# Kernel tuning notes

Hardware: AMD Instinct MI355X
Metric: run time of the kernel (lower is better)

The kernel has to match this reference:

```python
import jax, jax.numpy as jnp
import numpy as np

N_LAYERS = 2
N_ENT = 50000


def setup_inputs() -> dict:
    key = jax.random.key(0)
    k1, k2, k3, k4, k5 = jax.random.split(key, 5)
    R, N, D, E = 16, N_ENT, 128, 50000
    return {
        "ent_emb": jax.random.normal(k1, (N, D), dtype=jnp.float32),
        "rel_trans": jax.random.normal(k2, (R, D, D), dtype=jnp.float32) * (1.0 / np.sqrt(D)),
        "edge_val": jax.random.uniform(k3, (R, E), dtype=jnp.float32),
        "edge_row": jax.random.randint(k4, (R, E), 0, N, dtype=jnp.int32),
        "edge_col": jax.random.randint(k5, (R, E), 0, N, dtype=jnp.int32),
    }


def _spmm(row, col, val, emb):
    # out[i] = sum_{edges e with row[e]==i} val[e] * emb[col[e]]  (A @ emb)
    msgs = emb[col] * val[:, None]            # [E, d]
    return jax.ops.segment_sum(msgs, row, num_segments=N_ENT)  # [N, d]


def reference(ent_emb, rel_trans, edge_val, edge_row, edge_col):
    emb = ent_emb
    for _ in range(N_LAYERS):
        # per-relation sparse A_r @ emb -> [R, N, d]
        emb_acc = jax.vmap(_spmm, in_axes=(0, 0, 0, None))(edge_row, edge_col, edge_val, emb)
        # batched relation transform: rel_trans[r] @ emb_acc[r].T, transposed back
        tmp = jnp.einsum("rij,rnj->rni", rel_trans, emb_acc)  # [R, N, d]
        emb = jax.nn.relu(jnp.sum(tmp, axis=0))               # [N, d]
    # F.normalize: L2 along dim=1 with eps=1e-12
    norm = jnp.linalg.norm(emb, axis=1, keepdims=True)
    emb = emb / jnp.maximum(norm, 1e-12)
    return emb
```

## Files before the change

### kernel.cpp

```cpp
#include <hip/hip_runtime.h>
#include <stdint.h>

#define NE 50000
#define DD 128
#define RR 16
#define EE 50000
#define NT 64
#define NTOT (RR * NE)
#define SCAN_BLK 4096
#define NSCAN ((NTOT + SCAN_BLK - 1) / SCAN_BLK)

typedef short  shortx8 __attribute__((ext_vector_type(8)));
typedef short  shortx4 __attribute__((ext_vector_type(4)));
typedef float  floatx4 __attribute__((ext_vector_type(4)));

__device__ __forceinline__ unsigned short f2bf(float f) {
    unsigned u = __float_as_uint(f);
    u += 0x7fffu + ((u >> 16) & 1u);
    return (unsigned short)(u >> 16);
}
__device__ __forceinline__ float bf2f(unsigned short h) {
    return __uint_as_float(((unsigned)h) << 16);
}

#define ZB 782
#define TB 128
#define EB 6250
__global__ void prep_k(const float* __restrict__ rt, unsigned short* __restrict__ Tf,
                       const float4* __restrict__ emb, shortx4* __restrict__ embA,
                       int* __restrict__ counts) {
    int b = blockIdx.x, t = threadIdx.x;
    if (b < ZB) {
        int i4 = b * 256 + t;
        if (i4 < NTOT / 4) *(int4*)(counts + i4 * 4) = make_int4(0, 0, 0, 0);
    } else if (b < ZB + TB) {
        int c = (b - ZB) * 256 + t;
        int r = c >> 11, row = (c >> 4) & 127, cb = c & 15;
        int kt = cb >> 2, qq = cb & 3, rg = row >> 4, m = row & 15;
        const float4* src = (const float4*)(rt + (size_t)c * 8);
        float4 v0 = src[0], v1 = src[1];
        shortx8 w;
        w[0] = (short)f2bf(v0.x); w[1] = (short)f2bf(v0.y);
        w[2] = (short)f2bf(v0.z); w[3] = (short)f2bf(v0.w);
        w[4] = (short)f2bf(v1.x); w[5] = (short)f2bf(v1.y);
        w[6] = (short)f2bf(v1.z); w[7] = (short)f2bf(v1.w);
        size_t idx = ((((size_t)r * 8 + rg) * 4 + kt) * 64 + qq * 16 + m) * 8;
        *(shortx8*)(Tf + idx) = w;
    } else {
        int i = (b - ZB - TB) * 256 + t;
        if (i < NE * DD / 4) {
            float4 v = emb[i];
            shortx4 w;
            w[0] = (short)f2bf(v.x); w[1] = (short)f2bf(v.y);
            w[2] = (short)f2bf(v.z); w[3] = (short)f2bf(v.w);
            embA[i] = w;
        }
    }
}

__global__ void hist_k(const int* __restrict__ erow, int* __restrict__ counts,
                       uchar4* __restrict__ rank) {
    int r  = blockIdx.y;
    int i4 = blockIdx.x * 256 + threadIdx.x;
    if (i4 < EE / 4) {
        int4 rw = *(const int4*)(erow + (size_t)r * EE + i4 * 4);
        uchar4 rk;
        rk.x = (unsigned char)atomicAdd(&counts[rw.x * RR + r], 1);
        rk.y = (unsigned char)atomicAdd(&counts[rw.y * RR + r], 1);
        rk.z = (unsigned char)atomicAdd(&counts[rw.z * RR + r], 1);
        rk.w = (unsigned char)atomicAdd(&counts[rw.w * RR + r], 1);
        rank[(size_t)r * (EE / 4) + i4] = rk;
    }
}

__global__ void scanA(const int* __restrict__ c, int* __restrict__ bsum) {
    int b = blockIdx.x, t = threadIdx.x;
    int base = b * SCAN_BLK + t * 16;
    int s = 0;
    #pragma unroll
    for (int i = 0; i < 16; i++) {
        int idx = base + i;
        if (idx < NTOT) s += c[idx];
    }
    __shared__ int sh[256];
    sh[t] = s;
    __syncthreads();
    for (int off = 128; off > 0; off >>= 1) {
        if (t < off) sh[t] += sh[t + off];
        __syncthreads();
    }
    if (t == 0) bsum[b] = sh[0];
}

__global__ void scanC(const int* __restrict__ counts, int* __restrict__ rp,
                      const int* __restrict__ bsum) {
    int b = blockIdx.x, t = threadIdx.x;
    __shared__ int shb[256];
    shb[t] = (t < NSCAN) ? bsum[t] : 0;
    __syncthreads();
    for (int off = 1; off < 256; off <<= 1) {
        int add = (t >= off) ? shb[t - off] : 0;
        __syncthreads();
        shb[t] += add;
        __syncthreads();
    }
    int blockPrefix = (b > 0) ? shb[b - 1] : 0;
    int base = b * SCAN_BLK + t * 16;
    int vals[16];
    int s = 0;
    #pragma unroll
    for (int i = 0; i < 16; i++) {
        int idx = base + i;
        vals[i] = (idx < NTOT) ? counts[idx] : 0;
        s += vals[i];
    }
    __shared__ int sh[256];
    sh[t] = s;
    __syncthreads();
    for (int off = 1; off < 256; off <<= 1) {
        int add = (t >= off) ? sh[t - off] : 0;
        __syncthreads();
        sh[t] += add;
        __syncthreads();
    }
    int run = blockPrefix + sh[t] - s;
    #pragma unroll
    for (int i = 0; i < 16; i++) {
        int idx = base + i;
        if (idx < NTOT) {
            rp[idx] = run;
            run += vals[i];
            if (idx == NTOT - 1) rp[NTOT] = run;
        }
    }
}

__global__ void fill_k(const int* __restrict__ erow, const int* __restrict__ ecol,
                       const float* __restrict__ eval, const int* __restrict__ rp,
                       const uchar4* __restrict__ rank, int2* __restrict__ edges) {
    int r  = blockIdx.y;
    int i4 = blockIdx.x * 256 + threadIdx.x;
    if (i4 < EE / 4) {
        int4   rw = *(const int4*)(erow + (size_t)r * EE + i4 * 4);
        int4   cl = *(const int4*)(ecol + (size_t)r * EE + i4 * 4);
        float4 vl = *(const float4*)(eval + (size_t)r * EE + i4 * 4);
        uchar4 rk = rank[(size_t)r * (EE / 4) + i4];
        edges[rp[rw.x * RR + r] + rk.x] = make_int2(cl.x, __float_as_int(vl.x));
        edges[rp[rw.y * RR + r] + rk.y] = make_int2(cl.y, __float_as_int(vl.y));
        edges[rp[rw.z * RR + r] + rk.z] = make_int2(cl.z, __float_as_int(vl.z));
        edges[rp[rw.w * RR + r] + rk.w] = make_int2(cl.w, __float_as_int(vl.w));
    }
}

__device__ __forceinline__ void accum_chunks(float a0[8], float a1[8], float v,
                                             shortx8 c0, shortx8 c1) {
    #pragma unroll
    for (int j = 0; j < 8; j++) {
        a0[j] = fmaf(v, bf2f((unsigned short)c0[j]), a0[j]);
        a1[j] = fmaf(v, bf2f((unsigned short)c1[j]), a1[j]);
    }
}

template<bool FINAL>
__global__ __launch_bounds__(256, 4)
void layer_k(const unsigned short* __restrict__ embIn,
             const unsigned short* __restrict__ Tf,
             const int* __restrict__ rp,
             const int2* __restrict__ eg,
             unsigned short* __restrict__ embOut,
             float* __restrict__ outF)
{
    __shared__ __align__(16) unsigned short Bt[64 * 128];
    __shared__ float ssred[4][64];

    const int t    = threadIdx.x;
    const int lane = t & 63;
    const int w    = t >> 6;
    const int colq = lane & 15;
    const int q    = lane >> 4;
    const int n0   = blockIdx.x * NT;
    const int nsub = t >> 3;
    const int dgrp = t & 7;

    floatx4 acc[2][4];
    #pragma unroll
    for (int a = 0; a < 2; a++)
        #pragma unroll
        for (int c = 0; c < 4; c++)
            acc[a][c] = (floatx4){0.f, 0.f, 0.f, 0.f};

    #pragma unroll 1
    for (int r = 0; r < RR; r++) {
        int s_[2], c_[2];
        #pragma unroll
        for (int p = 0; p < 2; p++) {
            int n = n0 + p * 32 + nsub;
            bool ok = n < NE;
            int key = (ok ? n : 0) * RR + r;
            int a = rp[key], b2 = rp[key + 1];
            s_[p] = a; c_[p] = ok ? (b2 - a) : 0;
        }
        int   col0[2], col1[2];
        float v0_[2], v1_[2];
        #pragma unroll
        for (int p = 0; p < 2; p++) {
            int2 E0 = eg[s_[p]];
            int2 E1 = eg[s_[p] + 1];
            col0[p] = c_[p] > 0 ? E0.x : 0;
            col1[p] = c_[p] > 1 ? E1.x : 0;
            v0_[p]  = c_[p] > 0 ? __int_as_float(E0.y) : 0.f;
            v1_[p]  = c_[p] > 1 ? __int_as_float(E1.y) : 0.f;
        }
        shortx8 m[2][2][2];
        #pragma unroll
        for (int p = 0; p < 2; p++) {
            const unsigned short* r0 = embIn + (size_t)col0[p] * DD + dgrp * 8;
            const unsigned short* r1 = embIn + (size_t)col1[p] * DD + dgrp * 8;
            m[p][0][0] = *(const shortx8*)r0;
            m[p][0][1] = *(const shortx8*)(r0 + 64);
            m[p][1][0] = *(const shortx8*)r1;
            m[p][1][1] = *(const shortx8*)(r1 + 64);
        }
        #pragma unroll
        for (int p = 0; p < 2; p++) {
            float a0[8], a1[8];
            #pragma unroll
            for (int j = 0; j < 8; j++) { a0[j] = 0.f; a1[j] = 0.f; }
            accum_chunks(a0, a1, v0_[p], m[p][0][0], m[p][0][1]);
            accum_chunks(a0, a1, v1_[p], m[p][1][0], m[p][1][1]);
            if (c_[p] > 2) {
                #pragma unroll 1
                for (int k = s_[p] + 2; k < s_[p] + c_[p]; k++) {
                    int2 E = eg[k];
                    float v = __int_as_float(E.y);
                    const unsigned short* rw_ = embIn + (size_t)E.x * DD + dgrp * 8;
                    accum_chunks(a0, a1, v, *(const shortx8*)rw_, *(const shortx8*)(rw_ + 64));
                }
            }
            int nl = p * 32 + nsub;
            shortx8 w0, w1;
            #pragma unroll
            for (int j = 0; j < 8; j++) { w0[j] = (short)f2bf(a0[j]); w1[j] = (short)f2bf(a1[j]); }
            int pc = (dgrp ^ nl) & 7;
            *(shortx8*)&Bt[nl * 128 + pc * 8] = w0;
            *(shortx8*)&Bt[nl * 128 + (8 | pc) * 8] = w1;
        }
        __syncthreads();

        shortx8 afN[2];
        #pragma unroll
        for (int it2 = 0; it2 < 2; it2++)
            afN[it2] = *(const shortx8*)(Tf + ((((size_t)r * 8 + (w * 2 + it2)) * 4 + 0) * 64 + lane) * 8);
        #pragma unroll 1
        for (int kt = 0; kt < 4; kt++) {
            shortx8 afC[2];
            afC[0] = afN[0]; afC[1] = afN[1];
            if (kt < 3) {
                #pragma unroll
                for (int it2 = 0; it2 < 2; it2++)
                    afN[it2] = *(const shortx8*)(Tf + ((((size_t)r * 8 + (w * 2 + it2)) * 4 + (kt + 1)) * 64 + lane) * 8);
            }
            int lc = kt * 4 + q;
            shortx8 bfr[4];
            #pragma unroll
            for (int c = 0; c < 4; c++) {
                int nl = c * 16 + colq;
                int pc = (lc & 8) | ((lc ^ nl) & 7);
                bfr[c] = *(const shortx8*)&Bt[nl * 128 + pc * 8];
            }
            #pragma unroll
            for (int it2 = 0; it2 < 2; it2++)
                #pragma unroll
                for (int c = 0; c < 4; c++)
                    acc[it2][c] = __builtin_amdgcn_mfma_f32_16x16x32_bf16(afC[it2], bfr[c], acc[it2][c], 0, 0, 0);
        }
        __syncthreads();
    }

    if (!FINAL) {
        #pragma unroll
        for (int c = 0; c < 4; c++) {
            int n = n0 + c * 16 + colq;
            if (n < NE) {
                #pragma unroll
                for (int it2 = 0; it2 < 2; it2++) {
                    shortx4 wv;
                    #pragma unroll
                    for (int g = 0; g < 4; g++) {
                        float v = acc[it2][c][g];
                        v = v > 0.f ? v : 0.f;
                        wv[g] = (short)f2bf(v);
                    }
                    *(shortx4*)(embOut + ((size_t)n * DD + w * 32 + it2 * 16 + q * 4)) = wv;
                }
            }
        }
    } else {
        #pragma unroll
        for (int c = 0; c < 4; c++) {
            float ss = 0.f;
            #pragma unroll
            for (int it2 = 0; it2 < 2; it2++)
                #pragma unroll
                for (int g = 0; g < 4; g++) {
                    float v = acc[it2][c][g];
                    v = v > 0.f ? v : 0.f;
                    acc[it2][c][g] = v;
                    ss += v * v;
                }
            ss += __shfl_xor(ss, 16, 64);
            ss += __shfl_xor(ss, 32, 64);
            if (q == 0) ssred[w][c * 16 + colq] = ss;
        }
        __syncthreads();
        #pragma unroll
        for (int c = 0; c < 4; c++) {
            int nl = c * 16 + colq;
            float tot = ssred[0][nl] + ssred[1][nl] + ssred[2][nl] + ssred[3][nl];
            float scale = 1.f / fmaxf(sqrtf(tot), 1e-12f);
            int n = n0 + nl;
            if (n < NE) {
                #pragma unroll
                for (int it2 = 0; it2 < 2; it2++) {
                    floatx4 v4;
                    #pragma unroll
                    for (int g = 0; g < 4; g++) v4[g] = acc[it2][c][g] * scale;
                    *(floatx4*)(outF + ((size_t)n * DD + w * 32 + it2 * 16 + q * 4)) = v4;
                }
            }
        }
    }
}

static inline size_t align256(size_t x) { return (x + 255) & ~(size_t)255; }

extern "C" void kernel_launch(void* const* d_in, const int* in_sizes, int n_in,
                              void* d_out, int out_size, void* d_ws, size_t ws_size,
                              hipStream_t stream)
{
    const float* ent_emb   = (const float*)d_in[0];
    const float* rel_trans = (const float*)d_in[1];
    const float* edge_val  = (const float*)d_in[2];
    const int*   edge_row  = (const int*)d_in[3];
    const int*   edge_col  = (const int*)d_in[4];
    float* out = (float*)d_out;

    char* ws = (char*)d_ws;
    size_t off = 0;
    int* counts = (int*)(ws + off);  off = align256(off + (size_t)NTOT * 4);
    int* rpf    = (int*)(ws + off);  off = align256(off + ((size_t)NTOT + 1) * 4);
    int* bsum   = (int*)(ws + off);  off = align256(off + 256 * 4);
    uchar4* rank = (uchar4*)(ws + off); off = align256(off + (size_t)NTOT);
    int2* edges = (int2*)(ws + off); off = align256(off + ((size_t)NTOT + 4) * 8);
    unsigned short* Tf   = (unsigned short*)(ws + off); off = align256(off + (size_t)RR * DD * DD * 2);
    unsigned short* embA = (unsigned short*)(ws + off); off = align256(off + (size_t)NE * DD * 2);
    unsigned short* embB = (unsigned short*)(ws + off); off = align256(off + (size_t)NE * DD * 2);

    prep_k<<<ZB + TB + EB, 256, 0, stream>>>(rel_trans, Tf, (const float4*)ent_emb,
                                             (shortx4*)embA, counts);
    dim3 eg_grid((EE / 4 + 255) / 256, RR);
    hist_k<<<eg_grid, 256, 0, stream>>>(edge_row, counts, rank);
    scanA<<<NSCAN, 256, 0, stream>>>(counts, bsum);
    scanC<<<NSCAN, 256, 0, stream>>>(counts, rpf, bsum);
    fill_k<<<eg_grid, 256, 0, stream>>>(edge_row, edge_col, edge_val, rpf, rank, edges);

    int nb = (NE + NT - 1) / NT;
    layer_k<false><<<nb, 256, 0, stream>>>(embA, Tf, rpf, edges, embB, nullptr);
    layer_k<true ><<<nb, 256, 0, stream>>>(embB, Tf, rpf, edges, nullptr, out);
}
```

Measured before the change: 330.9 us.

## Double-buffer LDS tile and overlap next relation's gather with MFMA phase

Double-buffers the shared Bt tile so the sparse gather/accumulate for relation r+1 runs while the MFMA transform for relation r executes. Edge metadata is prefetched two relations ahead, and the first four edges per row are loaded up front instead of two. One barrier per iteration replaces two. Doubling LDS and lowering launch bounds to 3 blocks per SM reduces occupancy and raises register pressure in exchange for latency hiding.

```diff
diff --git a/kernel.cpp b/kernel.cpp
--- a/kernel.cpp
+++ b/kernel.cpp
@@ -162,7 +162,7 @@
 }
 
 template<bool FINAL>
-__global__ __launch_bounds__(256, 4)
+__global__ __launch_bounds__(256, 3)
 void layer_k(const unsigned short* __restrict__ embIn,
              const unsigned short* __restrict__ Tf,
              const int* __restrict__ rp,
@@ -170,7 +170,7 @@
              unsigned short* __restrict__ embOut,
              float* __restrict__ outF)
 {
-    __shared__ __align__(16) unsigned short Bt[64 * 128];
+    __shared__ __align__(16) unsigned short Bt[2][64 * 128];
     __shared__ float ssred[4][64];
 
     const int t    = threadIdx.x;
@@ -189,64 +189,39 @@
         for (int c = 0; c < 4; c++)
             acc[a][c] = (floatx4){0.f, 0.f, 0.f, 0.f};
 
-    #pragma unroll 1
-    for (int r = 0; r < RR; r++) {
-        int s_[2], c_[2];
+    struct EdgeMeta { int s[2], c[2]; int2 e0[2], e1[2]; };
+
+    auto metaEg = [&](int rr, EdgeMeta& st) {
         #pragma unroll
         for (int p = 0; p < 2; p++) {
             int n = n0 + p * 32 + nsub;
             bool ok = n < NE;
-            int key = (ok ? n : 0) * RR + r;
+            int key = (ok ? n : 0) * RR + rr;
             int a = rp[key], b2 = rp[key + 1];
-            s_[p] = a; c_[p] = ok ? (b2 - a) : 0;
-        }
-        int   col0[2], col1[2];
-        float v0_[2], v1_[2];
+            st.s[p] = a; st.c[p] = ok ? (b2 - a) : 0;
+            st.e0[p] = eg[a];
+            st.e1[p] = eg[a + 1];
+        }
+    };
+
+    auto embIssue = [&](const EdgeMeta& st, shortx8 (&mm)[2][2][2], float (&vv)[2][2]) {
         #pragma unroll
         for (int p = 0; p < 2; p++) {
-            int2 E0 = eg[s_[p]];
-            int2 E1 = eg[s_[p] + 1];
-            col0[p] = c_[p] > 0 ? E0.x : 0;
-            col1[p] = c_[p] > 1 ? E1.x : 0;
-            v0_[p]  = c_[p] > 0 ? __int_as_float(E0.y) : 0.f;
-            v1_[p]  = c_[p] > 1 ? __int_as_float(E1.y) : 0.f;
-        }
-        shortx8 m[2][2][2];
-        #pragma unroll
-        for (int p = 0; p < 2; p++) {
-            const unsigned short* r0 = embIn + (size_t)col0[p] * DD + dgrp * 8;
-            const unsigned short* r1 = embIn + (size_t)col1[p] * DD + dgrp * 8;
-            m[p][0][0] = *(const shortx8*)r0;
-            m[p][0][1] = *(const shortx8*)(r0 + 64);
-            m[p][1][0] = *(const shortx8*)r1;
-            m[p][1][1] = *(const shortx8*)(r1 + 64);
-        }
-        #pragma unroll
-        for (int p = 0; p < 2; p++) {
-            float a0[8], a1[8];
-            #pragma unroll
-            for (int j = 0; j < 8; j++) { a0[j] = 0.f; a1[j] = 0.f; }
-            accum_chunks(a0, a1, v0_[p], m[p][0][0], m[p][0][1]);
-            accum_chunks(a0, a1, v1_[p], m[p][1][0], m[p][1][1]);
-            if (c_[p] > 2) {
-                #pragma unroll 1
-                for (int k = s_[p] + 2; k < s_[p] + c_[p]; k++) {
-                    int2 E = eg[k];
-                    float v = __int_as_float(E.y);
-                    const unsigned short* rw_ = embIn + (size_t)E.x * DD + dgrp * 8;
-                    accum_chunks(a0, a1, v, *(const shortx8*)rw_, *(const shortx8*)(rw_ + 64));
-                }
-            }
-            int nl = p * 32 + nsub;
-            shortx8 w0, w1;
-            #pragma unroll
-            for (int j = 0; j < 8; j++) { w0[j] = (short)f2bf(a0[j]); w1[j] = (short)f2bf(a1[j]); }
-            int pc = (dgrp ^ nl) & 7;
-            *(shortx8*)&Bt[nl * 128 + pc * 8] = w0;
-            *(shortx8*)&Bt[nl * 128 + (8 | pc) * 8] = w1;
-        }
-        __syncthreads();
-
+            int col0 = st.c[p] > 0 ? st.e0[p].x : 0;
+            int col1 = st.c[p] > 1 ? st.e1[p].x : 0;
+            vv[p][0] = st.c[p] > 0 ? __int_as_float(st.e0[p].y) : 0.f;
+            vv[p][1] = st.c[p] > 1 ? __int_as_float(st.e1[p].y) : 0.f;
+            const unsigned short* r0 = embIn + (size_t)col0 * DD + dgrp * 8;
+            const unsigned short* r1 = embIn + (size_t)col1 * DD + dgrp * 8;
+            mm[p][0][0] = *(const shortx8*)r0;
+            mm[p][0][1] = *(const shortx8*)(r0 + 64);
+            mm[p][1][0] = *(const shortx8*)r1;
+            mm[p][1][1] = *(const shortx8*)(r1 + 64);
+        }
+    };
+
+    auto mfmaPhase = [&](int r) {
+        const unsigned short* bt = &Bt[r & 1][0];
         shortx8 afN[2];
         #pragma unroll
         for (int it2 = 0; it2 < 2; it2++)
@@ -266,7 +241,7 @@
             for (int c = 0; c < 4; c++) {
                 int nl = c * 16 + colq;
                 int pc = (lc & 8) | ((lc ^ nl) & 7);
-                bfr[c] = *(const shortx8*)&Bt[nl * 128 + pc * 8];
+                bfr[c] = *(const shortx8*)&bt[nl * 128 + pc * 8];
             }
             #pragma unroll
             for (int it2 = 0; it2 < 2; it2++)
@@ -274,8 +249,82 @@
                 for (int c = 0; c < 4; c++)
                     acc[it2][c] = __builtin_amdgcn_mfma_f32_16x16x32_bf16(afC[it2], bfr[c], acc[it2][c], 0, 0, 0);
         }
-        __syncthreads();
-    }
+    };
+
+    auto packPhase = [&](const EdgeMeta& st, shortx8 (&mm)[2][2][2], float (&vv)[2][2], int bsel) {
+        unsigned short* bt = &Bt[bsel][0];
+        int2 e2[2], e3[2];
+        #pragma unroll
+        for (int p = 0; p < 2; p++) {
+            e2[p] = eg[st.s[p] + 2];
+            e3[p] = eg[st.s[p] + 3];
+        }
+        shortx8 m2[2][2], m3[2][2];
+        float v2[2], v3[2];
+        #pragma unroll
+        for (int p = 0; p < 2; p++) {
+            int colF = st.c[p] > 0 ? st.e0[p].x : 0;
+            int col2 = st.c[p] > 2 ? e2[p].x : colF;
+            int col3 = st.c[p] > 3 ? e3[p].x : colF;
+            v2[p] = st.c[p] > 2 ? __int_as_float(e2[p].y) : 0.f;
+            v3[p] = st.c[p] > 3 ? __int_as_float(e3[p].y) : 0.f;
+            const unsigned short* r2 = embIn + (size_t)col2 * DD + dgrp * 8;
+            const unsigned short* r3 = embIn + (size_t)col3 * DD + dgrp * 8;
+            m2[p][0] = *(const shortx8*)r2;  m2[p][1] = *(const shortx8*)(r2 + 64);
+            m3[p][0] = *(const shortx8*)r3;  m3[p][1] = *(const shortx8*)(r3 + 64);
+        }
+        #pragma unroll
+        for (int p = 0; p < 2; p++) {
+            float a0[8], a1[8];
+            #pragma unroll
+            for (int j = 0; j < 8; j++) { a0[j] = 0.f; a1[j] = 0.f; }
+            accum_chunks(a0, a1, vv[p][0], mm[p][0][0], mm[p][0][1]);
+            accum_chunks(a0, a1, vv[p][1], mm[p][1][0], mm[p][1][1]);
+            accum_chunks(a0, a1, v2[p], m2[p][0], m2[p][1]);
+            accum_chunks(a0, a1, v3[p], m3[p][0], m3[p][1]);
+            if (st.c[p] > 4) {
+                #pragma unroll 1
+                for (int k = st.s[p] + 4; k < st.s[p] + st.c[p]; k++) {
+                    int2 E = eg[k];
+                    float v = __int_as_float(E.y);
+                    const unsigned short* rw_ = embIn + (size_t)E.x * DD + dgrp * 8;
+                    accum_chunks(a0, a1, v, *(const shortx8*)rw_, *(const shortx8*)(rw_ + 64));
+                }
+            }
+            int nl = p * 32 + nsub;
+            shortx8 w0, w1;
+            #pragma unroll
+            for (int j = 0; j < 8; j++) { w0[j] = (short)f2bf(a0[j]); w1[j] = (short)f2bf(a1[j]); }
+            int pc = (dgrp ^ nl) & 7;
+            *(shortx8*)&bt[nl * 128 + pc * 8] = w0;
+            *(shortx8*)&bt[nl * 128 + (8 | pc) * 8] = w1;
+        }
+    };
+
+    EdgeMeta sA, sB;
+    metaEg(0, sA);
+    metaEg(1, sB);
+    {
+        shortx8 mm[2][2][2]; float vv[2][2];
+        embIssue(sA, mm, vv);
+        packPhase(sA, mm, vv, 0);
+    }
+    asm volatile("s_waitcnt lgkmcnt(0)" ::: "memory");
+    __builtin_amdgcn_s_barrier();
+    sA = sB;
+
+    #pragma unroll 1
+    for (int r = 0; r < 15; r++) {
+        if (r < 14) metaEg(r + 2, sB);
+        shortx8 mm[2][2][2]; float vv[2][2];
+        embIssue(sA, mm, vv);
+        mfmaPhase(r);
+        packPhase(sA, mm, vv, (r + 1) & 1);
+        sA = sB;
+        asm volatile("s_waitcnt lgkmcnt(0)" ::: "memory");
+        __builtin_amdgcn_s_barrier();
+    }
+    mfmaPhase(15);
 
     if (!FINAL) {
         #pragma unroll
```

Measured after the change: 370.7 us. 1.12x slower.

## Prefetch next relation's edge metadata and gather four edges per row up front

Applied to the files above, without the earlier changes.

The layer kernel now loads the row-pointer range and the first four edge records for relation r+1 while relation r is being processed, carrying them across loop iterations in registers. It also issues embedding-row gathers for up to four edges at once instead of two, which adds memory-level parallelism for the irregular gathers. The __syncthreads calls become an explicit lgkmcnt wait plus s_barrier, so the barrier no longer waits on outstanding global loads. Occupancy is lowered from 4 to 3 blocks per SM to make room for the extra registers, and the edge buffer is padded so the speculative reads past the end stay in bounds.

```diff
diff --git a/kernel.cpp b/kernel.cpp
--- a/kernel.cpp
+++ b/kernel.cpp
@@ -162,7 +162,7 @@
 }
 
 template<bool FINAL>
-__global__ __launch_bounds__(256, 4)
+__global__ __launch_bounds__(256, 3)
 void layer_k(const unsigned short* __restrict__ embIn,
              const unsigned short* __restrict__ Tf,
              const int* __restrict__ rp,
@@ -189,52 +189,75 @@
         for (int c = 0; c < 4; c++)
             acc[a][c] = (floatx4){0.f, 0.f, 0.f, 0.f};
 
+    int s_[2], c_[2];
+    int2 E[2][4];
+    #pragma unroll
+    for (int p = 0; p < 2; p++) {
+        int n = n0 + p * 32 + nsub;
+        bool ok = n < NE;
+        int key = (ok ? n : 0) * RR;
+        int a = rp[key], b2 = rp[key + 1];
+        s_[p] = a; c_[p] = ok ? (b2 - a) : 0;
+        #pragma unroll
+        for (int e = 0; e < 4; e++) E[p][e] = eg[a + e];
+    }
+
     #pragma unroll 1
     for (int r = 0; r < RR; r++) {
-        int s_[2], c_[2];
+        shortx8 m[2][4][2];
+        float   v[2][4];
+        #pragma unroll
+        for (int p = 0; p < 2; p++) {
+            int col0 = c_[p] > 0 ? E[p][0].x : 0;
+            int col1 = c_[p] > 1 ? E[p][1].x : col0;
+            int col2 = c_[p] > 2 ? E[p][2].x : col0;
+            int col3 = c_[p] > 3 ? E[p][3].x : col0;
+            v[p][0] = c_[p] > 0 ? __int_as_float(E[p][0].y) : 0.f;
+            v[p][1] = c_[p] > 1 ? __int_as_float(E[p][1].y) : 0.f;
+            v[p][2] = __int_as_float(E[p][2].y);
+            v[p][3] = c_[p] > 3 ? __int_as_float(E[p][3].y) : 0.f;
+            const unsigned short* r0 = embIn + (size_t)col0 * DD + dgrp * 8;
+            const unsigned short* r1 = embIn + (size_t)col1 * DD + dgrp * 8;
+            const unsigned short* r2 = embIn + (size_t)col2 * DD + dgrp * 8;
+            const unsigned short* r3 = embIn + (size_t)col3 * DD + dgrp * 8;
+            m[p][0][0] = *(const shortx8*)r0;  m[p][0][1] = *(const shortx8*)(r0 + 64);
+            m[p][1][0] = *(const shortx8*)r1;  m[p][1][1] = *(const shortx8*)(r1 + 64);
+            m[p][2][0] = *(const shortx8*)r2;  m[p][2][1] = *(const shortx8*)(r2 + 64);
+            m[p][3][0] = *(const shortx8*)r3;  m[p][3][1] = *(const shortx8*)(r3 + 64);
+        }
+
+        int rn = (r + 1) & 15;
+        int sn[2], cn[2];
+        int2 En[2][4];
         #pragma unroll
         for (int p = 0; p < 2; p++) {
             int n = n0 + p * 32 + nsub;
             bool ok = n < NE;
-            int key = (ok ? n : 0) * RR + r;
+            int key = (ok ? n : 0) * RR + rn;
             int a = rp[key], b2 = rp[key + 1];
-            s_[p] = a; c_[p] = ok ? (b2 - a) : 0;
-        }
-        int   col0[2], col1[2];
-        float v0_[2], v1_[2];
-        #pragma unroll
-        for (int p = 0; p < 2; p++) {
-            int2 E0 = eg[s_[p]];
-            int2 E1 = eg[s_[p] + 1];
-            col0[p] = c_[p] > 0 ? E0.x : 0;
-            col1[p] = c_[p] > 1 ? E1.x : 0;
-            v0_[p]  = c_[p] > 0 ? __int_as_float(E0.y) : 0.f;
-            v1_[p]  = c_[p] > 1 ? __int_as_float(E1.y) : 0.f;
-        }
-        shortx8 m[2][2][2];
-        #pragma unroll
-        for (int p = 0; p < 2; p++) {
-            const unsigned short* r0 = embIn + (size_t)col0[p] * DD + dgrp * 8;
-            const unsigned short* r1 = embIn + (size_t)col1[p] * DD + dgrp * 8;
-            m[p][0][0] = *(const shortx8*)r0;
-            m[p][0][1] = *(const shortx8*)(r0 + 64);
-            m[p][1][0] = *(const shortx8*)r1;
-            m[p][1][1] = *(const shortx8*)(r1 + 64);
-        }
+            sn[p] = a; cn[p] = ok ? (b2 - a) : 0;
+            #pragma unroll
+            for (int e = 0; e < 4; e++) En[p][e] = eg[a + e];
+        }
+
         #pragma unroll
         for (int p = 0; p < 2; p++) {
             float a0[8], a1[8];
             #pragma unroll
             for (int j = 0; j < 8; j++) { a0[j] = 0.f; a1[j] = 0.f; }
-            accum_chunks(a0, a1, v0_[p], m[p][0][0], m[p][0][1]);
-            accum_chunks(a0, a1, v1_[p], m[p][1][0], m[p][1][1]);
+            accum_chunks(a0, a1, v[p][0], m[p][0][0], m[p][0][1]);
+            accum_chunks(a0, a1, v[p][1], m[p][1][0], m[p][1][1]);
             if (c_[p] > 2) {
+                accum_chunks(a0, a1, v[p][2], m[p][2][0], m[p][2][1]);
+                accum_chunks(a0, a1, v[p][3], m[p][3][0], m[p][3][1]);
+            }
+            if (c_[p] > 4) {
                 #pragma unroll 1
-                for (int k = s_[p] + 2; k < s_[p] + c_[p]; k++) {
-                    int2 E = eg[k];
-                    float v = __int_as_float(E.y);
-                    const unsigned short* rw_ = embIn + (size_t)E.x * DD + dgrp * 8;
-                    accum_chunks(a0, a1, v, *(const shortx8*)rw_, *(const shortx8*)(rw_ + 64));
+                for (int k = s_[p] + 4; k < s_[p] + c_[p]; k++) {
+                    int2 Et = eg[k];
+                    float vt = __int_as_float(Et.y);
+                    const unsigned short* rw_ = embIn + (size_t)Et.x * DD + dgrp * 8;
+                    accum_chunks(a0, a1, vt, *(const shortx8*)rw_, *(const shortx8*)(rw_ + 64));
                 }
             }
             int nl = p * 32 + nsub;
@@ -245,7 +268,8 @@
             *(shortx8*)&Bt[nl * 128 + pc * 8] = w0;
             *(shortx8*)&Bt[nl * 128 + (8 | pc) * 8] = w1;
         }
-        __syncthreads();
+        asm volatile("s_waitcnt lgkmcnt(0)" ::: "memory");
+        __builtin_amdgcn_s_barrier();
 
         shortx8 afN[2];
         #pragma unroll
@@ -265,8 +289,8 @@
             #pragma unroll
             for (int c = 0; c < 4; c++) {
                 int nl = c * 16 + colq;
-                int pc = (lc & 8) | ((lc ^ nl) & 7);
-                bfr[c] = *(const shortx8*)&Bt[nl * 128 + pc * 8];
+                int pcr = (lc & 8) | ((lc ^ nl) & 7);
+                bfr[c] = *(const shortx8*)&Bt[nl * 128 + pcr * 8];
             }
             #pragma unroll
             for (int it2 = 0; it2 < 2; it2++)
@@ -274,7 +298,15 @@
                 for (int c = 0; c < 4; c++)
                     acc[it2][c] = __builtin_amdgcn_mfma_f32_16x16x32_bf16(afC[it2], bfr[c], acc[it2][c], 0, 0, 0);
         }
-        __syncthreads();
+        asm volatile("s_waitcnt lgkmcnt(0)" ::: "memory");
+        __builtin_amdgcn_s_barrier();
+
+        #pragma unroll
+        for (int p = 0; p < 2; p++) {
+            s_[p] = sn[p]; c_[p] = cn[p];
+            #pragma unroll
+            for (int e = 0; e < 4; e++) E[p][e] = En[p][e];
+        }
     }
 
     if (!FINAL) {
@@ -287,9 +319,9 @@
                     shortx4 wv;
                     #pragma unroll
                     for (int g = 0; g < 4; g++) {
-                        float v = acc[it2][c][g];
-                        v = v > 0.f ? v : 0.f;
-                        wv[g] = (short)f2bf(v);
+                        float vv = acc[it2][c][g];
+                        vv = vv > 0.f ? vv : 0.f;
+                        wv[g] = (short)f2bf(vv);
                     }
                     *(shortx4*)(embOut + ((size_t)n * DD + w * 32 + it2 * 16 + q * 4)) = wv;
                 }
@@ -303,10 +335,10 @@
             for (int it2 = 0; it2 < 2; it2++)
                 #pragma unroll
                 for (int g = 0; g < 4; g++) {
-                    float v = acc[it2][c][g];
-                    v = v > 0.f ? v : 0.f;
-                    acc[it2][c][g] = v;
-                    ss += v * v;
+                    float vv = acc[it2][c][g];
+                    vv = vv > 0.f ? vv : 0.f;
+                    acc[it2][c][g] = vv;
+                    ss += vv * vv;
                 }
             ss += __shfl_xor(ss, 16, 64);
             ss += __shfl_xor(ss, 32, 64);
@@ -351,7 +383,7 @@
     int* rpf    = (int*)(ws + off);  off = align256(off + ((size_t)NTOT + 1) * 4);
     int* bsum   = (int*)(ws + off);  off = align256(off + 256 * 4);
     uchar4* rank = (uchar4*)(ws + off); off = align256(off + (size_t)NTOT);
-    int2* edges = (int2*)(ws + off); off = align256(off + ((size_t)NTOT + 4) * 8);
+    int2* edges = (int2*)(ws + off); off = align256(off + ((size_t)NTOT + 8) * 8);
     unsigned short* Tf   = (unsigned short*)(ws + off); off = align256(off + (size_t)RR * DD * DD * 2);
     unsigned short* embA = (unsigned short*)(ws + off); off = align256(off + (size_t)NE * DD * 2);
     unsigned short* embB = (unsigned short*)(ws + off); off = align256(off + (size_t)NE * DD * 2);
```

Measured after the change: 358.3 us. 8.3% more time.

## Split relations across two blocks per node tile, merging results with fp32 atomics

Applied to the files above, without the earlier changes.

Each layer launch now uses a 2D grid in which each block handles 8 of the 16 relations for a node tile. Partial results are merged with fp32 atomicAdd into zeroed accumulators. The second layer gathers fp32 rows and applies the ReLU on load. A separate kernel does the final ReLU and L2 normalization. The aim is to double the number of blocks so the GPU is filled better. The cost is atomic traffic, zeroing two fp32 buffers, and gathers twice as wide in layer two.

```diff
diff --git a/kernel.cpp b/kernel.cpp
--- a/kernel.cpp
+++ b/kernel.cpp
@@ -26,9 +26,10 @@
 #define ZB 782
 #define TB 128
 #define EB 6250
+#define DZ 3125
 __global__ void prep_k(const float* __restrict__ rt, unsigned short* __restrict__ Tf,
                        const float4* __restrict__ emb, shortx4* __restrict__ embA,
-                       int* __restrict__ counts) {
+                       int* __restrict__ counts, int4* __restrict__ dzero) {
     int b = blockIdx.x, t = threadIdx.x;
     if (b < ZB) {
         int i4 = b * 256 + t;
@@ -46,7 +47,7 @@
         w[6] = (short)f2bf(v1.z); w[7] = (short)f2bf(v1.w);
         size_t idx = ((((size_t)r * 8 + rg) * 4 + kt) * 64 + qq * 16 + m) * 8;
         *(shortx8*)(Tf + idx) = w;
-    } else {
+    } else if (b < ZB + TB + EB) {
         int i = (b - ZB - TB) * 256 + t;
         if (i < NE * DD / 4) {
             float4 v = emb[i];
@@ -55,6 +56,11 @@
             w[2] = (short)f2bf(v.z); w[3] = (short)f2bf(v.w);
             embA[i] = w;
         }
+    } else {
+        size_t base = (size_t)(b - ZB - TB - EB) * 1024 + t;
+        #pragma unroll
+        for (int k = 0; k < 4; k++)
+            dzero[base + k * 256] = make_int4(0, 0, 0, 0);
     }
 }
 
@@ -160,27 +166,43 @@
         a1[j] = fmaf(v, bf2f((unsigned short)c1[j]), a1[j]);
     }
 }
-
-template<bool FINAL>
+__device__ __forceinline__ void accum_f32(float a0[8], float a1[8], float v,
+                                          const float* rowp) {
+    floatx4 f0 = *(const floatx4*)(rowp);
+    floatx4 f1 = *(const floatx4*)(rowp + 4);
+    floatx4 f2 = *(const floatx4*)(rowp + 64);
+    floatx4 f3 = *(const floatx4*)(rowp + 68);
+    #pragma unroll
+    for (int j = 0; j < 4; j++) {
+        a0[j]     = fmaf(v, fmaxf(f0[j], 0.f), a0[j]);
+        a0[4 + j] = fmaf(v, fmaxf(f1[j], 0.f), a0[4 + j]);
+        a1[j]     = fmaf(v, fmaxf(f2[j], 0.f), a1[j]);
+        a1[4 + j] = fmaf(v, fmaxf(f3[j], 0.f), a1[4 + j]);
+    }
+}
+
+template<bool SRCF>
 __global__ __launch_bounds__(256, 4)
-void layer_k(const unsigned short* __restrict__ embIn,
+void layer_k(const void* __restrict__ srcP,
              const unsigned short* __restrict__ Tf,
              const int* __restrict__ rp,
              const int2* __restrict__ eg,
-             unsigned short* __restrict__ embOut,
-             float* __restrict__ outF)
+             float* __restrict__ Dout)
 {
     __shared__ __align__(16) unsigned short Bt[64 * 128];
-    __shared__ float ssred[4][64];
-
-    const int t    = threadIdx.x;
-    const int lane = t & 63;
-    const int w    = t >> 6;
-    const int colq = lane & 15;
-    const int q    = lane >> 4;
-    const int n0   = blockIdx.x * NT;
-    const int nsub = t >> 3;
-    const int dgrp = t & 7;
+
+    const unsigned short* embIn = (const unsigned short*)srcP;
+    const float*          fIn   = (const float*)srcP;
+
+    const int t     = threadIdx.x;
+    const int lane  = t & 63;
+    const int w     = t >> 6;
+    const int colq  = lane & 15;
+    const int q     = lane >> 4;
+    const int n0    = blockIdx.x * NT;
+    const int rbase = blockIdx.y * 8;
+    const int nsub  = t >> 3;
+    const int dgrp  = t & 7;
 
     floatx4 acc[2][4];
     #pragma unroll
@@ -190,7 +212,8 @@
             acc[a][c] = (floatx4){0.f, 0.f, 0.f, 0.f};
 
     #pragma unroll 1
-    for (int r = 0; r < RR; r++) {
+    for (int rr = 0; rr < 8; rr++) {
+        const int r = rbase + rr;
         int s_[2], c_[2];
         #pragma unroll
         for (int p = 0; p < 2; p++) {
@@ -211,30 +234,39 @@
             v0_[p]  = c_[p] > 0 ? __int_as_float(E0.y) : 0.f;
             v1_[p]  = c_[p] > 1 ? __int_as_float(E1.y) : 0.f;
         }
-        shortx8 m[2][2][2];
-        #pragma unroll
-        for (int p = 0; p < 2; p++) {
-            const unsigned short* r0 = embIn + (size_t)col0[p] * DD + dgrp * 8;
-            const unsigned short* r1 = embIn + (size_t)col1[p] * DD + dgrp * 8;
-            m[p][0][0] = *(const shortx8*)r0;
-            m[p][0][1] = *(const shortx8*)(r0 + 64);
-            m[p][1][0] = *(const shortx8*)r1;
-            m[p][1][1] = *(const shortx8*)(r1 + 64);
-        }
         #pragma unroll
         for (int p = 0; p < 2; p++) {
             float a0[8], a1[8];
             #pragma unroll
             for (int j = 0; j < 8; j++) { a0[j] = 0.f; a1[j] = 0.f; }
-            accum_chunks(a0, a1, v0_[p], m[p][0][0], m[p][0][1]);
-            accum_chunks(a0, a1, v1_[p], m[p][1][0], m[p][1][1]);
-            if (c_[p] > 2) {
-                #pragma unroll 1
-                for (int k = s_[p] + 2; k < s_[p] + c_[p]; k++) {
-                    int2 E = eg[k];
-                    float v = __int_as_float(E.y);
-                    const unsigned short* rw_ = embIn + (size_t)E.x * DD + dgrp * 8;
-                    accum_chunks(a0, a1, v, *(const shortx8*)rw_, *(const shortx8*)(rw_ + 64));
+            if constexpr (!SRCF) {
+                const unsigned short* r0 = embIn + (size_t)col0[p] * DD + dgrp * 8;
+                const unsigned short* r1 = embIn + (size_t)col1[p] * DD + dgrp * 8;
+                shortx8 m00 = *(const shortx8*)r0;
+                shortx8 m01 = *(const shortx8*)(r0 + 64);
+                shortx8 m10 = *(const shortx8*)r1;
+                shortx8 m11 = *(const shortx8*)(r1 + 64);
+                accum_chunks(a0, a1, v0_[p], m00, m01);
+                accum_chunks(a0, a1, v1_[p], m10, m11);
+                if (c_[p] > 2) {
+                    #pragma unroll 1
+                    for (int k = s_[p] + 2; k < s_[p] + c_[p]; k++) {
+                        int2 E = eg[k];
+                        float v = __int_as_float(E.y);
+                        const unsigned short* rw_ = embIn + (size_t)E.x * DD + dgrp * 8;
+                        accum_chunks(a0, a1, v, *(const shortx8*)rw_, *(const shortx8*)(rw_ + 64));
+                    }
+                }
+            } else {
+                accum_f32(a0, a1, v0_[p], fIn + (size_t)col0[p] * DD + dgrp * 8);
+                accum_f32(a0, a1, v1_[p], fIn + (size_t)col1[p] * DD + dgrp * 8);
+                if (c_[p] > 2) {
+                    #pragma unroll 1
+                    for (int k = s_[p] + 2; k < s_[p] + c_[p]; k++) {
+                        int2 E = eg[k];
+                        float v = __int_as_float(E.y);
+                        accum_f32(a0, a1, v, fIn + (size_t)E.x * DD + dgrp * 8);
+                    }
                 }
             }
             int nl = p * 32 + nsub;
@@ -265,8 +297,8 @@
             #pragma unroll
             for (int c = 0; c < 4; c++) {
                 int nl = c * 16 + colq;
-                int pc = (lc & 8) | ((lc ^ nl) & 7);
-                bfr[c] = *(const shortx8*)&Bt[nl * 128 + pc * 8];
+                int pcr = (lc & 8) | ((lc ^ nl) & 7);
+                bfr[c] = *(const shortx8*)&Bt[nl * 128 + pcr * 8];
             }
             #pragma unroll
             for (int it2 = 0; it2 < 2; it2++)
@@ -277,59 +309,43 @@
         __syncthreads();
     }
 
-    if (!FINAL) {
-        #pragma unroll
-        for (int c = 0; c < 4; c++) {
-            int n = n0 + c * 16 + colq;
-            if (n < NE) {
+    #pragma unroll
+    for (int c = 0; c < 4; c++) {
+        int n = n0 + c * 16 + colq;
+        if (n < NE) {
+            #pragma unroll
+            for (int it2 = 0; it2 < 2; it2++) {
+                float* dst = Dout + ((size_t)n * DD + w * 32 + it2 * 16 + q * 4);
                 #pragma unroll
-                for (int it2 = 0; it2 < 2; it2++) {
-                    shortx4 wv;
-                    #pragma unroll
-                    for (int g = 0; g < 4; g++) {
-                        float v = acc[it2][c][g];
-                        v = v > 0.f ? v : 0.f;
-                        wv[g] = (short)f2bf(v);
-                    }
-                    *(shortx4*)(embOut + ((size_t)n * DD + w * 32 + it2 * 16 + q * 4)) = wv;
-                }
+                for (int g = 0; g < 4; g++)
+                    atomicAdd(dst + g, acc[it2][c][g]);
             }
         }
-    } else {
-        #pragma unroll
-        for (int c = 0; c < 4; c++) {
-            float ss = 0.f;
-            #pragma unroll
-            for (int it2 = 0; it2 < 2; it2++)
-                #pragma unroll
-                for (int g = 0; g < 4; g++) {
-                    float v = acc[it2][c][g];
-                    v = v > 0.f ? v : 0.f;
-                    acc[it2][c][g] = v;
-                    ss += v * v;
-                }
-            ss += __shfl_xor(ss, 16, 64);
-            ss += __shfl_xor(ss, 32, 64);
-            if (q == 0) ssred[w][c * 16 + colq] = ss;
-        }
-        __syncthreads();
-        #pragma unroll
-        for (int c = 0; c < 4; c++) {
-            int nl = c * 16 + colq;
-            float tot = ssred[0][nl] + ssred[1][nl] + ssred[2][nl] + ssred[3][nl];
-            float scale = 1.f / fmaxf(sqrtf(tot), 1e-12f);
-            int n = n0 + nl;
-            if (n < NE) {
-                #pragma unroll
-                for (int it2 = 0; it2 < 2; it2++) {
-                    floatx4 v4;
-                    #pragma unroll
-                    for (int g = 0; g < 4; g++) v4[g] = acc[it2][c][g] * scale;
-                    *(floatx4*)(outF + ((size_t)n * DD + w * 32 + it2 * 16 + q * 4)) = v4;
-                }
-            }
-        }
-    }
+    }
+}
+
+__global__ __launch_bounds__(256)
+void final_k(const float* __restrict__ Dacc, float* __restrict__ out) {
+    int t = threadIdx.x;
+    int node = blockIdx.x * 8 + (t >> 5);
+    int l = t & 31;
+    floatx4 v = *(const floatx4*)(Dacc + (size_t)node * DD + l * 4);
+    float ss = 0.f;
+    #pragma unroll
+    for (int g = 0; g < 4; g++) {
+        v[g] = v[g] > 0.f ? v[g] : 0.f;
+        ss += v[g] * v[g];
+    }
+    ss += __shfl_xor(ss, 1,  64);
+    ss += __shfl_xor(ss, 2,  64);
+    ss += __shfl_xor(ss, 4,  64);
+    ss += __shfl_xor(ss, 8,  64);
+    ss += __shfl_xor(ss, 16, 64);
+    float scale = 1.f / fmaxf(sqrtf(ss), 1e-12f);
+    floatx4 o;
+    #pragma unroll
+    for (int g = 0; g < 4; g++) o[g] = v[g] * scale;
+    *(floatx4*)(out + (size_t)node * DD + l * 4) = o;
 }
 
 static inline size_t align256(size_t x) { return (x + 255) & ~(size_t)255; }
@@ -351,20 +367,22 @@
     int* rpf    = (int*)(ws + off);  off = align256(off + ((size_t)NTOT + 1) * 4);
     int* bsum   = (int*)(ws + off);  off = align256(off + 256 * 4);
     uchar4* rank = (uchar4*)(ws + off); off = align256(off + (size_t)NTOT);
-    int2* edges = (int2*)(ws + off); off = align256(off + ((size_t)NTOT + 4) * 8);
-    unsigned short* Tf   = (unsigned short*)(ws + off); off = align256(off + (size_t)RR * DD * DD * 2);
+    int2* edges = (int2*)(ws + off); off = align256(off + ((size_t)NTOT + 8) * 8);
+    unsigned short* Tf = (unsigned short*)(ws + off); off = align256(off + (size_t)RR * DD * DD * 2);
     unsigned short* embA = (unsigned short*)(ws + off); off = align256(off + (size_t)NE * DD * 2);
-    unsigned short* embB = (unsigned short*)(ws + off); off = align256(off + (size_t)NE * DD * 2);
-
-    prep_k<<<ZB + TB + EB, 256, 0, stream>>>(rel_trans, Tf, (const float4*)ent_emb,
-                                             (shortx4*)embA, counts);
+    float* Dacc0 = (float*)(ws + off); off = align256(off + (size_t)NE * DD * 4);
+    float* Dacc1 = (float*)(ws + off); off = align256(off + (size_t)NE * DD * 4);
+
+    prep_k<<<ZB + TB + EB + DZ, 256, 0, stream>>>(rel_trans, Tf, (const float4*)ent_emb,
+                                                  (shortx4*)embA, counts, (int4*)Dacc0);
     dim3 eg_grid((EE / 4 + 255) / 256, RR);
     hist_k<<<eg_grid, 256, 0, stream>>>(edge_row, counts, rank);
     scanA<<<NSCAN, 256, 0, stream>>>(counts, bsum);
     scanC<<<NSCAN, 256, 0, stream>>>(counts, rpf, bsum);
     fill_k<<<eg_grid, 256, 0, stream>>>(edge_row, edge_col, edge_val, rpf, rank, edges);
 
-    int nb = (NE + NT - 1) / NT;
-    layer_k<false><<<nb, 256, 0, stream>>>(embA, Tf, rpf, edges, embB, nullptr);
-    layer_k<true ><<<nb, 256, 0, stream>>>(embB, Tf, rpf, edges, nullptr, out);
-}
+    dim3 lay_grid((NE + NT - 1) / NT, 2);
+    layer_k<false><<<lay_grid, 256, 0, stream>>>(embA,  Tf, rpf, edges, Dacc0);
+    layer_k<true ><<<lay_grid, 256, 0, stream>>>(Dacc0, Tf, rpf, edges, Dacc1);
+    final_k<<<NE / 8, 256, 0, stream>>>(Dacc1, out);
+}
```

After: 604.5 us. 82.7% more time.
